# Kernel optimization log

Hardware: AMD Instinct MI355X
Metric: run time of the kernel (lower is better)

Reference implementation:

```python
import jax, jax.numpy as jnp
import numpy as np

B, S, T, D, V, H = 8, 256, 128, 768, 50257, 12
HD = D // H
TAU = 0.5
RATE = 1.0
PARAM1, PARAM2 = 0.0, 1.0  # n_step=0 => param2=1, param1=0 (update happens after use)
NEG = -1e9


def gru_cell(x, h, w_ih, w_hh, b_ih, b_hh):
    # torch nn.GRU cell math
    gi = x @ w_ih.T + b_ih   # [B,3D]
    gh = h @ w_hh.T + b_hh   # [B,3D]
    i_r, i_z, i_n = jnp.split(gi, 3, axis=-1)
    h_r, h_z, h_n = jnp.split(gh, 3, axis=-1)
    r = jax.nn.sigmoid(i_r + h_r)
    z = jax.nn.sigmoid(i_z + h_z)
    n = jnp.tanh(i_n + r * h_n)
    return (1.0 - z) * n + z * h


def gru_scan(x_btd, h0, lens, w_ih, w_hh, b_ih, b_hh):
    # emulates packed GRU: hidden frozen past each length, outputs zero past length
    x_tbd = jnp.swapaxes(x_btd, 0, 1)
    ts = jnp.arange(x_tbd.shape[0])
    def step(h, xt_t):
        xt, t = xt_t
        hn = gru_cell(xt, h, w_ih, w_hh, b_ih, b_hh)
        valid = (t < lens)[:, None]
        hn = jnp.where(valid, hn, h)
        out = jnp.where(valid, hn, 0.0)
        return hn, out
    hT, outs = jax.lax.scan(step, h0, (x_tbd, ts))
    return hT, jnp.swapaxes(outs, 0, 1)


def decay_attn(tgt, mem, mem_lens, in_w, in_b, ow, ob):
    # nn.MultiheadAttention with key_padding_mask; y = tgt + rate*attn(tgt, mem, mem)
    b, s, _ = tgt.shape
    t = mem.shape[1]
    q = (tgt @ in_w[:D].T + in_b[:D]).reshape(b, s, H, HD)
    k = (mem @ in_w[D:2 * D].T + in_b[D:2 * D]).reshape(b, t, H, HD)
    v = (mem @ in_w[2 * D:].T + in_b[2 * D:]).reshape(b, t, H, HD)
    scores = jnp.einsum('bshd,bthd->bhst', q, k) / np.sqrt(HD)
    pad = jnp.arange(t)[None, :] >= mem_lens[:, None]  # True at padding
    scores = jnp.where(pad[:, None, None, :], NEG, scores)
    a = jax.nn.softmax(scores, axis=-1)
    o = jnp.einsum('bhst,bthd->bshd', a, v).reshape(b, s, D)
    o = o @ ow.T + ob
    return tgt + RATE * o


def setup_inputs() -> dict:
    key = jax.random.key(0)
    ks = jax.random.split(key, 24)
    w = lambda k, shape: jax.random.normal(k, shape, jnp.float32) * 0.02
    src = jax.random.randint(ks[0], (B, S), 0, V)
    dst = jax.random.randint(ks[1], (B, T), 0, V)
    src_len = jax.random.randint(ks[2], (B,), 1, S + 1).at[0].set(S)
    dst_len = jax.random.randint(ks[3], (B,), 1, T + 1).at[0].set(T)
    u = jax.random.uniform(ks[4], (T - 1, B, D), jnp.float32, 1e-6, 1.0 - 1e-6)
    gumbel = -jnp.log(-jnp.log(u))
    return dict(
        src=src, src_len=src_len, dst=dst, dst_len=dst_len,
        wte=w(ks[5], (V, D)),
        enc_w_ih=w(ks[6], (3 * D, D)), enc_w_hh=w(ks[7], (3 * D, D)),
        enc_b_ih=jnp.zeros((3 * D,), jnp.float32), enc_b_hh=jnp.zeros((3 * D,), jnp.float32),
        dec_w_ih=w(ks[8], (3 * D, D)), dec_w_hh=w(ks[9], (3 * D, D)),
        dec_b_ih=jnp.zeros((3 * D,), jnp.float32), dec_b_hh=jnp.zeros((3 * D,), jnp.float32),
        out_w=w(ks[10], (V, D)), out_b=jnp.zeros((V,), jnp.float32),
        ll_w=w(ks[11], (D, D)), ll_b=jnp.zeros((D,), jnp.float32),
        attn_in_w=w(ks[12], (3 * D, D)), attn_in_b=jnp.zeros((3 * D,), jnp.float32),
        attn_out_w=w(ks[13], (D, D)), attn_out_b=jnp.zeros((D,), jnp.float32),
        gumbel=gumbel,
    )


def reference(src, src_len, dst, dst_len, wte,
              enc_w_ih, enc_w_hh, enc_b_ih, enc_b_hh,
              dec_w_ih, dec_w_hh, dec_b_ih, dec_b_hh,
              out_w, out_b, ll_w, ll_b,
              attn_in_w, attn_in_b, attn_out_w, attn_out_b, gumbel):
    src_e = wte[src]  # [B,S,D]
    dst_e = wte[dst]  # [B,T,D]

    # first encode of src (packed GRU -> final hidden)
    h_enc, _ = gru_scan(src_e, jnp.zeros((B, D), src_e.dtype), src_len,
                        enc_w_ih, enc_w_hh, enc_b_ih, enc_b_hh)

    # scheduled-sampling decode (select_rate=0 => always oracle branch)
    h0 = gru_cell(dst_e[:, 0], h_enc, dec_w_ih, dec_w_hh, dec_b_ih, dec_b_hh)
    def step(h, g):
        y_soft = jax.nn.softmax((h + g) / TAU, axis=-1)  # gumbel-softmax over D
        oracle = jnp.argmax(y_soft, axis=-1)             # ids in [0, D)
        x = wte[oracle]
        hn = gru_cell(x, h, dec_w_ih, dec_w_hh, dec_b_ih, dec_b_hh)
        return hn, hn
    _, hs = jax.lax.scan(step, h0, gumbel)
    final_output = jnp.swapaxes(jnp.concatenate([h0[None], hs], axis=0), 0, 1)  # [B,T,D]

    cand_logits = final_output @ out_w.T + out_b          # [B,T,V]
    cand = wte[jnp.argmax(cand_logits, axis=-1)]          # [B,T,D]

    c_output = decay_attn(src_e, cand, dst_len, attn_in_w, attn_in_b, attn_out_w, attn_out_b)
    c_aft = src_e @ ll_w.T + ll_b
    c_multi = PARAM1 * c_aft + PARAM2 * c_output

    h_enc2, _ = gru_scan(c_multi, jnp.zeros((B, D), c_multi.dtype), src_len,
                         enc_w_ih, enc_w_hh, enc_b_ih, enc_b_hh)
    _, dst_out = gru_scan(dst_e, h_enc2, dst_len,
                          dec_w_ih, dec_w_hh, dec_b_ih, dec_b_hh)  # [B,T,D], zero-padded
    y = dst_out @ out_w.T + out_b                          # [B,T,V]
    latent_loss = jnp.sum((c_aft - c_output) ** 2)
    return (y, latent_loss)
```

## Files before the change

kernel.cpp:

```cpp
#include <hip/hip_runtime.h>

typedef unsigned short u16;
typedef unsigned int   u32;
typedef unsigned long long u64;
typedef __attribute__((ext_vector_type(8))) short short8;
typedef __attribute__((ext_vector_type(4))) float floatx4;

#define B_ 8
#define S_ 256
#define T_ 128
#define D_ 768
#define G3 2304
#define V_ 50257
#define SCAN_BLOCKS 96

__device__ __forceinline__ u16 f2bf(float f){
  u32 u = __builtin_bit_cast(u32, f);
  u32 r = (u + 0x7fffu + ((u >> 16) & 1u)) >> 16;
  return (u16)r;
}
__device__ __forceinline__ u32 fkey(float f){
  u32 u = __builtin_bit_cast(u32, f);
  return (u & 0x80000000u) ? ~u : (u | 0x80000000u);
}

__device__ __forceinline__ float pick4(float x0, float x1, float x2, float x3, int i){
  return i == 0 ? x0 : i == 1 ? x1 : i == 2 ? x2 : x3;
}

__device__ __forceinline__ float gru_h(float gir, float giz, float gin,
                                       float hr, float hz_, float hn, float hold){
  float r = 1.f / (1.f + expf(-(gir + hr)));
  float z = 1.f / (1.f + expf(-(giz + hz_)));
  float n = tanhf(gin + r * hn);
  return (1.f - z) * n + z * hold;
}

__device__ __forceinline__ void bar_sync(int* ctr, int nb, int target){
  __syncthreads();
  if (threadIdx.x == 0){
    int c = __hip_atomic_fetch_add(ctr, 1, __ATOMIC_RELAXED, __HIP_MEMORY_SCOPE_AGENT);
    if (c + 1 < target){
      int spins = 0;
      while (__hip_atomic_load(ctr, __ATOMIC_RELAXED, __HIP_MEMORY_SCOPE_AGENT) < target){
        __builtin_amdgcn_s_sleep(1);
        if (++spins > (1 << 17)) break;
      }
    }
  }
  __syncthreads();
}

__global__ __launch_bounds__(256) void embed_kernel(
    const int* __restrict__ src, const int* __restrict__ dst, const float* __restrict__ wte,
    float* __restrict__ src_e, u16* __restrict__ src_ebf, u16* __restrict__ dst_ebf,
    u16* __restrict__ wte768_bf)
{
  int row = blockIdx.x;
  if (row < B_*S_){
    const float* wp = wte + (size_t)src[row] * D_;
    for (int c = threadIdx.x; c < D_; c += 256){
      float w = wp[c];
      src_e[(size_t)row*D_ + c] = w;
      src_ebf[(size_t)row*D_ + c] = f2bf(w);
    }
  } else if (row < B_*S_ + B_*T_){
    int r2 = row - B_*S_;
    const float* wp = wte + (size_t)dst[r2] * D_;
    for (int c = threadIdx.x; c < D_; c += 256) dst_ebf[(size_t)r2*D_ + c] = f2bf(wp[c]);
  } else {
    int r3 = row - (B_*S_ + B_*T_);
    const float* wp = wte + (size_t)r3 * D_;
    for (int c = threadIdx.x; c < D_; c += 256) wte768_bf[(size_t)r3*D_ + c] = f2bf(wp[c]);
  }
}

__global__ __launch_bounds__(256) void gemm_kernel(
    const u16* __restrict__ A, const float* __restrict__ Bm, const float* __restrict__ bias,
    float* __restrict__ outF, u16* __restrict__ outBF, const float* __restrict__ resid,
    u64* __restrict__ amax, int M, int N, int K)
{
  __shared__ __align__(16) u16 As[128][40];
  __shared__ __align__(16) u16 Bs[128][40];
  const int tid = threadIdx.x;
  const int m0 = blockIdx.y * 128, n0 = blockIdx.x * 128;
  const int lrow = tid >> 2, lk = (tid & 3) * 8;
  const int lane = tid & 63, wv = tid >> 6;
  const int wm = (wv & 1) * 64, wn = (wv >> 1) * 64;
  const int quad = lane >> 4, l16 = lane & 15;
  floatx4 acc[4][4];
  #pragma unroll
  for (int i = 0; i < 4; i++)
    #pragma unroll
    for (int jj = 0; jj < 4; jj++){
      acc[i][jj][0] = 0.f; acc[i][jj][1] = 0.f; acc[i][jj][2] = 0.f; acc[i][jj][3] = 0.f;
    }

  const int n1 = n0 + lrow;
  for (int k0 = 0; k0 < K; k0 += 32){
    __syncthreads();
    *(uint4*)&As[lrow][lk]    = *(const uint4*)(A + (size_t)(m0 + lrow)      * K + k0 + lk);
    *(uint4*)&As[lrow+64][lk] = *(const uint4*)(A + (size_t)(m0 + lrow + 64) * K + k0 + lk);
    #pragma unroll
    for (int half = 0; half < 2; half++){
      const int nr = n1 + half*64;
      short8 pk = {0,0,0,0,0,0,0,0};
      if (nr < N){
        const float4* bp = (const float4*)(Bm + (size_t)nr * K + k0 + lk);
        float4 b0 = bp[0], b1 = bp[1];
        pk[0] = (short)f2bf(b0.x); pk[1] = (short)f2bf(b0.y);
        pk[2] = (short)f2bf(b0.z); pk[3] = (short)f2bf(b0.w);
        pk[4] = (short)f2bf(b1.x); pk[5] = (short)f2bf(b1.y);
        pk[6] = (short)f2bf(b1.z); pk[7] = (short)f2bf(b1.w);
      }
      *(short8*)&Bs[lrow + half*64][lk] = pk;
    }
    __syncthreads();
    short8 af[4], bf[4];
    #pragma unroll
    for (int i = 0; i < 4; i++)  af[i] = *(const short8*)&As[wm + i*16 + l16][quad*8];
    #pragma unroll
    for (int jj = 0; jj < 4; jj++) bf[jj] = *(const short8*)&Bs[wn + jj*16 + l16][quad*8];
    #pragma unroll
    for (int i = 0; i < 4; i++)
      #pragma unroll
      for (int jj = 0; jj < 4; jj++)
        acc[i][jj] = __builtin_amdgcn_mfma_f32_16x16x32_bf16(af[i], bf[jj], acc[i][jj], 0, 0, 0);
  }

  #pragma unroll
  for (int i = 0; i < 4; i++){
    #pragma unroll
    for (int r = 0; r < 4; r++){
      const int m = m0 + wm + i*16 + quad*4 + r;
      u64 best = 0;
      #pragma unroll
      for (int jj = 0; jj < 4; jj++){
        const int n = n0 + wn + jj*16 + l16;
        if (n < N){
          float vv = acc[i][jj][r];
          if (bias)  vv += bias[n];
          if (resid) vv += resid[(size_t)m * N + n];
          if (outF)  outF[(size_t)m * N + n] = vv;
          if (outBF) outBF[(size_t)m * N + n] = f2bf(vv);
          if (amax){
            u64 p = ((u64)fkey(vv) << 32) | (u64)(0xFFFFFFFFu - (u32)n);
            if (p > best) best = p;
          }
        }
      }
      if (amax){
        #pragma unroll
        for (int msk = 1; msk < 16; msk <<= 1){
          u64 o = __shfl_xor(best, msk, 64);
          if (o > best) best = o;
        }
        if (l16 == 0) atomicMax(&amax[m], best);
      }
    }
  }
}

__global__ __launch_bounds__(256, 1) void gru_scan_kernel(
    const float* __restrict__ gi, const float* __restrict__ w_hh, const float* __restrict__ b_hh,
    const float* __restrict__ h_in, float* __restrict__ hA, float* __restrict__ hB,
    float* __restrict__ h_out, u16* __restrict__ out_bf, const int* __restrict__ lens,
    int steps, int* bar)
{
  __shared__ __align__(16) float h_lds[B_ * D_];
  const int tid = threadIdx.x, lane = tid & 63, wv = tid >> 6;
  const int grp = lane >> 5, s = lane & 31;
  const int j0 = blockIdx.x * 8 + wv * 2;
  float w[2][3][24];
  #pragma unroll
  for (int c = 0; c < 2; c++)
    #pragma unroll
    for (int g = 0; g < 3; g++){
      const float* p = w_hh + ((size_t)(g * D_ + j0 + c)) * D_ + s;
      #pragma unroll
      for (int i = 0; i < 24; i++) w[c][g][i] = p[i * 32];
    }
  const bool fin = (s < 8);
  const int fbb = s >> 1, fc = s & 1;
  const int fb = grp * 4 + fbb, fj = j0 + fc;
  const float br = b_hh[fj], bz = b_hh[D_ + fj], bn = b_hh[2 * D_ + fj];
  const int len_b = lens ? lens[fb] : 0x7fffffff;
  const int nb = gridDim.x;
  const float* cur = h_in;
  float* nxt = hA;
  int bc = 0;
  for (int t = 0; t < steps; t++){
    float g0 = 0.f, g1 = 0.f, g2 = 0.f;
    if (fin){
      const float* gp = gi + ((size_t)fb * steps + t) * G3;
      g0 = gp[fj]; g1 = gp[D_ + fj]; g2 = gp[2 * D_ + fj];
    }
    #pragma unroll
    for (int i = 0; i < 12; i++){
      const int idx = tid + i * 256;
      u64 v = __hip_atomic_load((const u64*)cur + idx, __ATOMIC_RELAXED, __HIP_MEMORY_SCOPE_AGENT);
      *((u64*)h_lds + idx) = v;
    }
    __syncthreads();
    float acc[2][3][4];
    #pragma unroll
    for (int c = 0; c < 2; c++)
      #pragma unroll
      for (int g = 0; g < 3; g++)
        #pragma unroll
        for (int bb = 0; bb < 4; bb++) acc[c][g][bb] = 0.f;
    #pragma unroll
    for (int i = 0; i < 24; i++){
      const int k = s + i * 32;
      #pragma unroll
      for (int bb = 0; bb < 4; bb++){
        const float hv = h_lds[(grp * 4 + bb) * D_ + k];
        #pragma unroll
        for (int c = 0; c < 2; c++){
          acc[c][0][bb] += w[c][0][i] * hv;
          acc[c][1][bb] += w[c][1][i] * hv;
          acc[c][2][bb] += w[c][2][i] * hv;
        }
      }
    }
    #pragma unroll
    for (int m = 1; m < 32; m <<= 1){
      #pragma unroll
      for (int c = 0; c < 2; c++)
        #pragma unroll
        for (int g = 0; g < 3; g++)
          #pragma unroll
          for (int bb = 0; bb < 4; bb++)
            acc[c][g][bb] += __shfl_xor(acc[c][g][bb], m, 64);
    }
    if (fin){
      const float sr = fc ? pick4(acc[1][0][0], acc[1][0][1], acc[1][0][2], acc[1][0][3], fbb)
                          : pick4(acc[0][0][0], acc[0][0][1], acc[0][0][2], acc[0][0][3], fbb);
      const float sz = fc ? pick4(acc[1][1][0], acc[1][1][1], acc[1][1][2], acc[1][1][3], fbb)
                          : pick4(acc[0][1][0], acc[0][1][1], acc[0][1][2], acc[0][1][3], fbb);
      const float sn = fc ? pick4(acc[1][2][0], acc[1][2][1], acc[1][2][2], acc[1][2][3], fbb)
                          : pick4(acc[0][2][0], acc[0][2][1], acc[0][2][2], acc[0][2][3], fbb);
      const float hold = h_lds[fb * D_ + fj];
      const float hn_ = gru_h(g0, g1, g2, sr + br, sz + bz, sn + bn, hold);
      const bool valid = (t < len_b);
      const float hnew = valid ? hn_ : hold;
      __hip_atomic_store(nxt + fb * D_ + fj, hnew, __ATOMIC_RELAXED, __HIP_MEMORY_SCOPE_AGENT);
      if (out_bf) out_bf[((size_t)fb * steps + t) * D_ + fj] = f2bf(valid ? hn_ : 0.f);
      if (h_out && t == steps - 1) h_out[fb * D_ + fj] = hnew;
    }
    bar_sync(bar, nb, nb * (++bc));
    const float* c2 = nxt; nxt = (nxt == hA) ? hB : hA; cur = c2;
  }
}

__global__ __launch_bounds__(256, 1) void gru_decode_kernel(
    const float* __restrict__ gi3, const float* __restrict__ E, const float* __restrict__ gumbel,
    const float* __restrict__ w_hh, const float* __restrict__ b_hh,
    const float* __restrict__ h_in, float* __restrict__ hA, float* __restrict__ hB,
    u16* __restrict__ fo_bf, int* bar)
{
  __shared__ __align__(16) float h_lds[B_ * D_];
  __shared__ int oracle[B_];
  const int tid = threadIdx.x, lane = tid & 63, wv = tid >> 6;
  const int grp = lane >> 5, s = lane & 31;
  const int j0 = blockIdx.x * 8 + wv * 2;
  float w[2][3][24];
  #pragma unroll
  for (int c = 0; c < 2; c++)
    #pragma unroll
    for (int g = 0; g < 3; g++){
      const float* p = w_hh + ((size_t)(g * D_ + j0 + c)) * D_ + s;
      #pragma unroll
      for (int i = 0; i < 24; i++) w[c][g][i] = p[i * 32];
    }
  const bool fin = (s < 8);
  const int fbb = s >> 1, fc = s & 1;
  const int fb = grp * 4 + fbb, fj = j0 + fc;
  const float br = b_hh[fj], bz = b_hh[D_ + fj], bn = b_hh[2 * D_ + fj];
  const int nb = gridDim.x;
  const float* cur = h_in;
  float* nxt = hA;
  int bc = 0;
  for (int t = 0; t < T_; t++){
    #pragma unroll
    for (int i = 0; i < 12; i++){
      const int idx = tid + i * 256;
      u64 v = __hip_atomic_load((const u64*)cur + idx, __ATOMIC_RELAXED, __HIP_MEMORY_SCOPE_AGENT);
      *((u64*)h_lds + idx) = v;
    }
    __syncthreads();
    if (t > 0){
      #pragma unroll
      for (int rep = 0; rep < 2; rep++){
        const int b = wv * 2 + rep;
        const float* gp = gumbel + ((size_t)(t - 1) * B_ + b) * D_;
        u64 best = 0;
        #pragma unroll
        for (int i = 0; i < 12; i++){
          const int d = lane + i * 64;
          const float v = h_lds[b * D_ + d] + gp[d];
          u64 p = ((u64)fkey(v) << 32) | (u64)(0xFFFFFFFFu - (u32)d);
          if (p > best) best = p;
        }
        #pragma unroll
        for (int msk = 1; msk < 64; msk <<= 1){
          u64 o = __shfl_xor(best, msk, 64);
          if (o > best) best = o;
        }
        if (lane == 0) oracle[b] = (int)(0xFFFFFFFFu - (u32)(best & 0xFFFFFFFFull));
      }
    }
    __syncthreads();
    float g0 = 0.f, g1 = 0.f, g2 = 0.f;
    if (fin){
      const float* gp = (t == 0) ? (gi3 + (size_t)fb * T_ * G3) : (E + (size_t)oracle[fb] * G3);
      g0 = gp[fj]; g1 = gp[D_ + fj]; g2 = gp[2 * D_ + fj];
    }
    float acc[2][3][4];
    #pragma unroll
    for (int c = 0; c < 2; c++)
      #pragma unroll
      for (int g = 0; g < 3; g++)
        #pragma unroll
        for (int bb = 0; bb < 4; bb++) acc[c][g][bb] = 0.f;
    #pragma unroll
    for (int i = 0; i < 24; i++){
      const int k = s + i * 32;
      #pragma unroll
      for (int bb = 0; bb < 4; bb++){
        const float hv = h_lds[(grp * 4 + bb) * D_ + k];
        #pragma unroll
        for (int c = 0; c < 2; c++){
          acc[c][0][bb] += w[c][0][i] * hv;
          acc[c][1][bb] += w[c][1][i] * hv;
          acc[c][2][bb] += w[c][2][i] * hv;
        }
      }
    }
    #pragma unroll
    for (int m = 1; m < 32; m <<= 1){
      #pragma unroll
      for (int c = 0; c < 2; c++)
        #pragma unroll
        for (int g = 0; g < 3; g++)
          #pragma unroll
          for (int bb = 0; bb < 4; bb++)
            acc[c][g][bb] += __shfl_xor(acc[c][g][bb], m, 64);
    }
    if (fin){
      const float sr = fc ? pick4(acc[1][0][0], acc[1][0][1], acc[1][0][2], acc[1][0][3], fbb)
                          : pick4(acc[0][0][0], acc[0][0][1], acc[0][0][2], acc[0][0][3], fbb);
      const float sz = fc ? pick4(acc[1][1][0], acc[1][1][1], acc[1][1][2], acc[1][1][3], fbb)
                          : pick4(acc[0][1][0], acc[0][1][1], acc[0][1][2], acc[0][1][3], fbb);
      const float sn = fc ? pick4(acc[1][2][0], acc[1][2][1], acc[1][2][2], acc[1][2][3], fbb)
                          : pick4(acc[0][2][0], acc[0][2][1], acc[0][2][2], acc[0][2][3], fbb);
      const float hold = h_lds[fb * D_ + fj];
      const float hn_ = gru_h(g0, g1, g2, sr + br, sz + bz, sn + bn, hold);
      __hip_atomic_store(nxt + fb * D_ + fj, hn_, __ATOMIC_RELAXED, __HIP_MEMORY_SCOPE_AGENT);
      fo_bf[((size_t)fb * T_ + t) * D_ + fj] = f2bf(hn_);
    }
    bar_sync(bar, nb, nb * (++bc));
    const float* c2 = nxt; nxt = (nxt == hA) ? hB : hA; cur = c2;
  }
}

__global__ __launch_bounds__(256) void cand_gather_kernel(
    const u64* __restrict__ amax, const float* __restrict__ wte, u16* __restrict__ cand_bf)
{
  int row = blockIdx.x;
  u32 n = 0xFFFFFFFFu - (u32)(amax[row] & 0xFFFFFFFFull);
  if (n >= (u32)V_) n = 0;
  const float* wp = wte + (size_t)n * D_;
  for (int c = threadIdx.x; c < D_; c += 256) cand_bf[(size_t)row*D_ + c] = f2bf(wp[c]);
}

__global__ __launch_bounds__(64) void attn_kernel(
    const float* __restrict__ q, const float* __restrict__ k, const float* __restrict__ v,
    const int* __restrict__ dlen, u16* __restrict__ ao_bf)
{
  __shared__ __align__(16) float qs[64];
  __shared__ float al[128];
  const int lane = threadIdx.x;
  const int hh = blockIdx.x, s = blockIdx.y, b = blockIdx.z;
  qs[lane] = q[((size_t)(b*S_ + s))*D_ + hh*64 + lane];
  __syncthreads();
  const int len = dlen[b];
  float sc0 = -1e9f, sc1 = -1e9f;
  #pragma unroll
  for (int r = 0; r < 2; r++){
    int t = lane + r*64;
    if (t < len){
      const float4* kp = (const float4*)(k + ((size_t)(b*T_ + t))*D_ + hh*64);
      float acc = 0.f;
      #pragma unroll
      for (int i = 0; i < 16; i++){
        float4 kv = kp[i];
        float4 qv = *((const float4*)qs + i);
        acc += qv.x*kv.x + qv.y*kv.y + qv.z*kv.z + qv.w*kv.w;
      }
      if (r == 0) sc0 = acc * 0.125f; else sc1 = acc * 0.125f;
    }
  }
  float mx = fmaxf(sc0, sc1);
  #pragma unroll
  for (int msk = 1; msk < 64; msk <<= 1) mx = fmaxf(mx, __shfl_xor(mx, msk, 64));
  float e0 = (sc0 > -1e8f) ? expf(sc0 - mx) : 0.f;
  float e1 = (sc1 > -1e8f) ? expf(sc1 - mx) : 0.f;
  float sm = e0 + e1;
  #pragma unroll
  for (int msk = 1; msk < 64; msk <<= 1) sm += __shfl_xor(sm, msk, 64);
  float inv = 1.f / sm;
  al[lane] = e0 * inv; al[lane + 64] = e1 * inv;
  __syncthreads();
  float o = 0.f;
  #pragma unroll 4
  for (int t = 0; t < T_; t++) o += al[t] * v[((size_t)(b*T_ + t))*D_ + hh*64 + lane];
  ao_bf[((size_t)(b*S_ + s))*D_ + hh*64 + lane] = f2bf(o);
}

__global__ __launch_bounds__(256) void loss_kernel(
    const float* __restrict__ a, const float* __restrict__ c, float* __restrict__ acc, int n)
{
  float s = 0.f;
  for (int i = blockIdx.x*256 + threadIdx.x; i < n; i += gridDim.x*256){
    float d = a[i] - c[i]; s += d*d;
  }
  #pragma unroll
  for (int msk = 1; msk < 64; msk <<= 1) s += __shfl_xor(s, msk, 64);
  __shared__ float ps[4];
  if ((threadIdx.x & 63) == 0) ps[threadIdx.x >> 6] = s;
  __syncthreads();
  if (threadIdx.x == 0) atomicAdd(acc, ps[0] + ps[1] + ps[2] + ps[3]);
}

__global__ void loss_write_kernel(const float* __restrict__ acc, float* __restrict__ out){
  if (threadIdx.x == 0 && blockIdx.x == 0) out[0] = *acc;
}

extern "C" void kernel_launch(void* const* d_in, const int* in_sizes, int n_in,
                              void* d_out, int out_size, void* d_ws, size_t ws_size,
                              hipStream_t stream)
{
  (void)in_sizes; (void)n_in;
  const int*   src      = (const int*)d_in[0];
  const int*   src_len  = (const int*)d_in[1];
  const int*   dst      = (const int*)d_in[2];
  const int*   dst_len  = (const int*)d_in[3];
  const float* wte      = (const float*)d_in[4];
  const float* enc_w_ih = (const float*)d_in[5];
  const float* enc_w_hh = (const float*)d_in[6];
  const float* enc_b_ih = (const float*)d_in[7];
  const float* enc_b_hh = (const float*)d_in[8];
  const float* dec_w_ih = (const float*)d_in[9];
  const float* dec_w_hh = (const float*)d_in[10];
  const float* dec_b_ih = (const float*)d_in[11];
  const float* dec_b_hh = (const float*)d_in[12];
  const float* out_w    = (const float*)d_in[13];
  const float* out_b    = (const float*)d_in[14];
  const float* ll_w     = (const float*)d_in[15];
  const float* ll_b     = (const float*)d_in[16];
  const float* attn_in_w  = (const float*)d_in[17];
  const float* attn_in_b  = (const float*)d_in[18];
  const float* attn_out_w = (const float*)d_in[19];
  const float* attn_out_b = (const float*)d_in[20];
  const float* gumbel   = (const float*)d_in[21];

  unsigned char* base = (unsigned char*)d_ws;
  size_t off = 0;
  auto alloc = [&](size_t bytes) -> void* {
    off = (off + 255) & ~(size_t)255;
    void* p = base + off; off += bytes; return p;
  };
  int*   bar      = (int*)alloc(256);
  u64*   amax     = (u64*)alloc((size_t)(B_*T_)*8);
  float* hz       = (float*)alloc((size_t)B_*D_*4);
  float* hA       = (float*)alloc((size_t)B_*D_*4);
  float* hB       = (float*)alloc((size_t)B_*D_*4);
  float* h_enc    = (float*)alloc((size_t)B_*D_*4);
  float* h_enc2   = (float*)alloc((size_t)B_*D_*4);
  float* src_e    = (float*)alloc((size_t)B_*S_*D_*4);
  u16*   src_ebf  = (u16*)alloc((size_t)B_*S_*D_*2);
  u16*   dst_ebf  = (u16*)alloc((size_t)B_*T_*D_*2);
  u16*   wte768   = (u16*)alloc((size_t)D_*D_*2);
  float* gi3      = (float*)alloc((size_t)B_*T_*G3*4);
  u16*   fo_bf    = (u16*)alloc((size_t)B_*T_*D_*2);
  u16*   cand_bf  = (u16*)alloc((size_t)B_*T_*D_*2);
  u16*   ao_bf    = (u16*)alloc((size_t)B_*S_*D_*2);
  u16*   cm_bf    = (u16*)alloc((size_t)B_*S_*D_*2);
  u16*   do_bf    = (u16*)alloc((size_t)B_*T_*D_*2);
  float* BIG      = (float*)alloc((size_t)B_*S_*G3*4);
  float* gi12  = BIG;
  float* Em    = BIG;
  float* qf    = BIG;
  float* kf    = BIG + (size_t)B_*S_*D_;
  float* vf    = kf  + (size_t)B_*T_*D_;
  float* c_out = vf  + (size_t)B_*T_*D_;
  float* c_aft = BIG;
  float* lossAcc = (float*)(bar + 8);

  const size_t needed = off;
  if (ws_size < needed) return;

  hipMemsetAsync(bar, 0, 256, stream);
  hipMemsetAsync(amax, 0, (size_t)(B_*T_)*8, stream);
  hipMemsetAsync(hz, 0, (size_t)B_*D_*4, stream);

  auto gemm = [&](const u16* A, const float* Bw, const float* bias, float* oF, u16* oB,
                  const float* resid, u64* am, int M, int N, int K){
    dim3 g((unsigned)((N + 127) / 128), (unsigned)(M / 128));
    gemm_kernel<<<g, 256, 0, stream>>>(A, Bw, bias, oF, oB, resid, am, M, N, K);
  };

  embed_kernel<<<B_*S_ + B_*T_ + D_, 256, 0, stream>>>(src, dst, wte, src_e, src_ebf,
                                                       dst_ebf, wte768);

  gemm(src_ebf, enc_w_ih, enc_b_ih, gi12, nullptr, nullptr, nullptr, B_*S_, G3, D_);
  gru_scan_kernel<<<SCAN_BLOCKS, 256, 0, stream>>>(gi12, enc_w_hh, enc_b_hh, hz, hA, hB,
                                                   h_enc, nullptr, src_len, S_, bar + 0);
  gemm(dst_ebf, dec_w_ih, dec_b_ih, gi3, nullptr, nullptr, nullptr, B_*T_, G3, D_);
  gemm(wte768, dec_w_ih, dec_b_ih, Em, nullptr, nullptr, nullptr, D_, G3, D_);
  gru_decode_kernel<<<SCAN_BLOCKS, 256, 0, stream>>>(gi3, Em, gumbel, dec_w_hh, dec_b_hh,
                                                     h_enc, hA, hB, fo_bf, bar + 2);
  gemm(fo_bf, out_w, out_b, nullptr, nullptr, nullptr, amax, B_*T_, V_, D_);
  cand_gather_kernel<<<B_*T_, 256, 0, stream>>>(amax, wte, cand_bf);
  gemm(src_ebf, attn_in_w,                    attn_in_b,        qf, nullptr, nullptr, nullptr, B_*S_, D_, D_);
  gemm(cand_bf, attn_in_w + (size_t)D_*D_,    attn_in_b + D_,   kf, nullptr, nullptr, nullptr, B_*T_, D_, D_);
  gemm(cand_bf, attn_in_w + (size_t)2*D_*D_,  attn_in_b + 2*D_, vf, nullptr, nullptr, nullptr, B_*T_, D_, D_);
  attn_kernel<<<dim3(12, S_, B_), 64, 0, stream>>>(qf, kf, vf, dst_len, ao_bf);
  gemm(ao_bf, attn_out_w, attn_out_b, c_out, cm_bf, src_e, nullptr, B_*S_, D_, D_);
  gemm(src_ebf, ll_w, ll_b, c_aft, nullptr, nullptr, nullptr, B_*S_, D_, D_);
  loss_kernel<<<1024, 256, 0, stream>>>(c_aft, c_out, lossAcc, B_*S_*D_);
  gemm(cm_bf, enc_w_ih, enc_b_ih, gi12, nullptr, nullptr, nullptr, B_*S_, G3, D_);
  gru_scan_kernel<<<SCAN_BLOCKS, 256, 0, stream>>>(gi12, enc_w_hh, enc_b_hh, hz, hA, hB,
                                                   h_enc2, nullptr, src_len, S_, bar + 4);
  gru_scan_kernel<<<SCAN_BLOCKS, 256, 0, stream>>>(gi3, dec_w_hh, dec_b_hh, h_enc2, hA, hB,
                                                   nullptr, do_bf, dst_len, T_, bar + 6);
  gemm(do_bf, out_w, out_b, (float*)d_out, nullptr, nullptr, nullptr, B_*T_, V_, D_);
  loss_write_kernel<<<1, 64, 0, stream>>>(lossAcc, (float*)d_out + (size_t)out_size - 1);
}
```

Before: 8.868 ms.

## Halve GRU scan grid with 512-thread blocks and per-block flag barrier

The persistent GRU scan and decode kernels now run 48 blocks of 512 threads, each owning 16 hidden columns, instead of 96 blocks of 256 threads. The single atomic-counter grid barrier is replaced by per-block flag slots that every block polls in parallel. Both changes aim to cut per-step grid synchronisation latency, which dominates these sequential loops. The cost is more waves per CU with register-resident weights, and a barrier workspace enlarged to hold the flags.

```diff
diff --git a/kernel.cpp b/kernel.cpp
--- a/kernel.cpp
+++ b/kernel.cpp
@@ -12,7 +12,8 @@
 #define D_ 768
 #define G3 2304
 #define V_ 50257
-#define SCAN_BLOCKS 96
+#define SCAN_BLOCKS 48
+#define SCAN_THREADS 512
 
 __device__ __forceinline__ u16 f2bf(float f){
   u32 u = __builtin_bit_cast(u32, f);
@@ -36,16 +37,16 @@
   return (1.f - z) * n + z * hold;
 }
 
-__device__ __forceinline__ void bar_sync(int* ctr, int nb, int target){
+__device__ __forceinline__ void flag_bar(int* flags, int nb, int bc){
   __syncthreads();
-  if (threadIdx.x == 0){
-    int c = __hip_atomic_fetch_add(ctr, 1, __ATOMIC_RELAXED, __HIP_MEMORY_SCOPE_AGENT);
-    if (c + 1 < target){
-      int spins = 0;
-      while (__hip_atomic_load(ctr, __ATOMIC_RELAXED, __HIP_MEMORY_SCOPE_AGENT) < target){
-        __builtin_amdgcn_s_sleep(1);
-        if (++spins > (1 << 17)) break;
-      }
+  const int tid = threadIdx.x;
+  if (tid == 0)
+    __hip_atomic_store(&flags[blockIdx.x], bc, __ATOMIC_RELAXED, __HIP_MEMORY_SCOPE_AGENT);
+  if (tid < nb){
+    int spins = 0;
+    while (__hip_atomic_load(&flags[tid], __ATOMIC_RELAXED, __HIP_MEMORY_SCOPE_AGENT) < bc){
+      __builtin_amdgcn_s_sleep(1);
+      if (++spins > (1 << 17)) break;
     }
   }
   __syncthreads();
@@ -161,16 +162,16 @@
   }
 }
 
-__global__ __launch_bounds__(256, 1) void gru_scan_kernel(
+__global__ __launch_bounds__(SCAN_THREADS, 1) void gru_scan_kernel(
     const float* __restrict__ gi, const float* __restrict__ w_hh, const float* __restrict__ b_hh,
     const float* __restrict__ h_in, float* __restrict__ hA, float* __restrict__ hB,
     float* __restrict__ h_out, u16* __restrict__ out_bf, const int* __restrict__ lens,
-    int steps, int* bar)
+    int steps, int* flags)
 {
   __shared__ __align__(16) float h_lds[B_ * D_];
   const int tid = threadIdx.x, lane = tid & 63, wv = tid >> 6;
   const int grp = lane >> 5, s = lane & 31;
-  const int j0 = blockIdx.x * 8 + wv * 2;
+  const int j0 = blockIdx.x * 16 + wv * 2;
   float w[2][3][24];
   #pragma unroll
   for (int c = 0; c < 2; c++)
@@ -188,7 +189,6 @@
   const int nb = gridDim.x;
   const float* cur = h_in;
   float* nxt = hA;
-  int bc = 0;
   for (int t = 0; t < steps; t++){
     float g0 = 0.f, g1 = 0.f, g2 = 0.f;
     if (fin){
@@ -196,8 +196,8 @@
       g0 = gp[fj]; g1 = gp[D_ + fj]; g2 = gp[2 * D_ + fj];
     }
     #pragma unroll
-    for (int i = 0; i < 12; i++){
-      const int idx = tid + i * 256;
+    for (int i = 0; i < 6; i++){
+      const int idx = tid + i * SCAN_THREADS;
       u64 v = __hip_atomic_load((const u64*)cur + idx, __ATOMIC_RELAXED, __HIP_MEMORY_SCOPE_AGENT);
       *((u64*)h_lds + idx) = v;
     }
@@ -248,22 +248,22 @@
       if (out_bf) out_bf[((size_t)fb * steps + t) * D_ + fj] = f2bf(valid ? hn_ : 0.f);
       if (h_out && t == steps - 1) h_out[fb * D_ + fj] = hnew;
     }
-    bar_sync(bar, nb, nb * (++bc));
+    flag_bar(flags, nb, t + 1);
     const float* c2 = nxt; nxt = (nxt == hA) ? hB : hA; cur = c2;
   }
 }
 
-__global__ __launch_bounds__(256, 1) void gru_decode_kernel(
+__global__ __launch_bounds__(SCAN_THREADS, 1) void gru_decode_kernel(
     const float* __restrict__ gi3, const float* __restrict__ E, const float* __restrict__ gumbel,
     const float* __restrict__ w_hh, const float* __restrict__ b_hh,
     const float* __restrict__ h_in, float* __restrict__ hA, float* __restrict__ hB,
-    u16* __restrict__ fo_bf, int* bar)
+    u16* __restrict__ fo_bf, int* flags)
 {
   __shared__ __align__(16) float h_lds[B_ * D_];
   __shared__ int oracle[B_];
   const int tid = threadIdx.x, lane = tid & 63, wv = tid >> 6;
   const int grp = lane >> 5, s = lane & 31;
-  const int j0 = blockIdx.x * 8 + wv * 2;
+  const int j0 = blockIdx.x * 16 + wv * 2;
   float w[2][3][24];
   #pragma unroll
   for (int c = 0; c < 2; c++)
@@ -280,35 +280,31 @@
   const int nb = gridDim.x;
   const float* cur = h_in;
   float* nxt = hA;
-  int bc = 0;
   for (int t = 0; t < T_; t++){
     #pragma unroll
-    for (int i = 0; i < 12; i++){
-      const int idx = tid + i * 256;
+    for (int i = 0; i < 6; i++){
+      const int idx = tid + i * SCAN_THREADS;
       u64 v = __hip_atomic_load((const u64*)cur + idx, __ATOMIC_RELAXED, __HIP_MEMORY_SCOPE_AGENT);
       *((u64*)h_lds + idx) = v;
     }
     __syncthreads();
     if (t > 0){
-      #pragma unroll
-      for (int rep = 0; rep < 2; rep++){
-        const int b = wv * 2 + rep;
-        const float* gp = gumbel + ((size_t)(t - 1) * B_ + b) * D_;
-        u64 best = 0;
-        #pragma unroll
-        for (int i = 0; i < 12; i++){
-          const int d = lane + i * 64;
-          const float v = h_lds[b * D_ + d] + gp[d];
-          u64 p = ((u64)fkey(v) << 32) | (u64)(0xFFFFFFFFu - (u32)d);
-          if (p > best) best = p;
-        }
-        #pragma unroll
-        for (int msk = 1; msk < 64; msk <<= 1){
-          u64 o = __shfl_xor(best, msk, 64);
-          if (o > best) best = o;
-        }
-        if (lane == 0) oracle[b] = (int)(0xFFFFFFFFu - (u32)(best & 0xFFFFFFFFull));
-      }
+      const int b = wv;
+      const float* gp = gumbel + ((size_t)(t - 1) * B_ + b) * D_;
+      u64 best = 0;
+      #pragma unroll
+      for (int i = 0; i < 12; i++){
+        const int d = lane + i * 64;
+        const float v = h_lds[b * D_ + d] + gp[d];
+        u64 p = ((u64)fkey(v) << 32) | (u64)(0xFFFFFFFFu - (u32)d);
+        if (p > best) best = p;
+      }
+      #pragma unroll
+      for (int msk = 1; msk < 64; msk <<= 1){
+        u64 o = __shfl_xor(best, msk, 64);
+        if (o > best) best = o;
+      }
+      if (lane == 0) oracle[b] = (int)(0xFFFFFFFFu - (u32)(best & 0xFFFFFFFFull));
     }
     __syncthreads();
     float g0 = 0.f, g1 = 0.f, g2 = 0.f;
@@ -359,7 +355,7 @@
       __hip_atomic_store(nxt + fb * D_ + fj, hn_, __ATOMIC_RELAXED, __HIP_MEMORY_SCOPE_AGENT);
       fo_bf[((size_t)fb * T_ + t) * D_ + fj] = f2bf(hn_);
     }
-    bar_sync(bar, nb, nb * (++bc));
+    flag_bar(flags, nb, t + 1);
     const float* c2 = nxt; nxt = (nxt == hA) ? hB : hA; cur = c2;
   }
 }
@@ -471,7 +467,7 @@
     off = (off + 255) & ~(size_t)255;
     void* p = base + off; off += bytes; return p;
   };
-  int*   bar      = (int*)alloc(256);
+  int*   bar      = (int*)alloc(1280);
   u64*   amax     = (u64*)alloc((size_t)(B_*T_)*8);
   float* hz       = (float*)alloc((size_t)B_*D_*4);
   float* hA       = (float*)alloc((size_t)B_*D_*4);
@@ -496,12 +492,12 @@
   float* vf    = kf  + (size_t)B_*T_*D_;
   float* c_out = vf  + (size_t)B_*T_*D_;
   float* c_aft = BIG;
-  float* lossAcc = (float*)(bar + 8);
+  float* lossAcc = (float*)(bar + 256);
 
   const size_t needed = off;
   if (ws_size < needed) return;
 
-  hipMemsetAsync(bar, 0, 256, stream);
+  hipMemsetAsync(bar, 0, 1280, stream);
   hipMemsetAsync(amax, 0, (size_t)(B_*T_)*8, stream);
   hipMemsetAsync(hz, 0, (size_t)B_*D_*4, stream);
 
@@ -515,12 +511,12 @@
                                                        dst_ebf, wte768);
 
   gemm(src_ebf, enc_w_ih, enc_b_ih, gi12, nullptr, nullptr, nullptr, B_*S_, G3, D_);
-  gru_scan_kernel<<<SCAN_BLOCKS, 256, 0, stream>>>(gi12, enc_w_hh, enc_b_hh, hz, hA, hB,
-                                                   h_enc, nullptr, src_len, S_, bar + 0);
+  gru_scan_kernel<<<SCAN_BLOCKS, SCAN_THREADS, 0, stream>>>(gi12, enc_w_hh, enc_b_hh, hz, hA, hB,
+                                                            h_enc, nullptr, src_len, S_, bar + 0);
   gemm(dst_ebf, dec_w_ih, dec_b_ih, gi3, nullptr, nullptr, nullptr, B_*T_, G3, D_);
   gemm(wte768, dec_w_ih, dec_b_ih, Em, nullptr, nullptr, nullptr, D_, G3, D_);
-  gru_decode_kernel<<<SCAN_BLOCKS, 256, 0, stream>>>(gi3, Em, gumbel, dec_w_hh, dec_b_hh,
-                                                     h_enc, hA, hB, fo_bf, bar + 2);
+  gru_decode_kernel<<<SCAN_BLOCKS, SCAN_THREADS, 0, stream>>>(gi3, Em, gumbel, dec_w_hh, dec_b_hh,
+                                                              h_enc, hA, hB, fo_bf, bar + 64);
   gemm(fo_bf, out_w, out_b, nullptr, nullptr, nullptr, amax, B_*T_, V_, D_);
   cand_gather_kernel<<<B_*T_, 256, 0, stream>>>(amax, wte, cand_bf);
   gemm(src_ebf, attn_in_w,                    attn_in_b,        qf, nullptr, nullptr, nullptr, B_*S_, D_, D_);
@@ -531,10 +527,10 @@
   gemm(src_ebf, ll_w, ll_b, c_aft, nullptr, nullptr, nullptr, B_*S_, D_, D_);
   loss_kernel<<<1024, 256, 0, stream>>>(c_aft, c_out, lossAcc, B_*S_*D_);
   gemm(cm_bf, enc_w_ih, enc_b_ih, gi12, nullptr, nullptr, nullptr, B_*S_, G3, D_);
-  gru_scan_kernel<<<SCAN_BLOCKS, 256, 0, stream>>>(gi12, enc_w_hh, enc_b_hh, hz, hA, hB,
-                                                   h_enc2, nullptr, src_len, S_, bar + 4);
-  gru_scan_kernel<<<SCAN_BLOCKS, 256, 0, stream>>>(gi3, dec_w_hh, dec_b_hh, h_enc2, hA, hB,
-                                                   nullptr, do_bf, dst_len, T_, bar + 6);
+  gru_scan_kernel<<<SCAN_BLOCKS, SCAN_THREADS, 0, stream>>>(gi12, enc_w_hh, enc_b_hh, hz, hA, hB,
+                                                            h_enc2, nullptr, src_len, S_, bar + 128);
+  gru_scan_kernel<<<SCAN_BLOCKS, SCAN_THREADS, 0, stream>>>(gi3, dec_w_hh, dec_b_hh, h_enc2, hA, hB,
+                                                            nullptr, do_bf, dst_len, T_, bar + 192);
   gemm(do_bf, out_w, out_b, (float*)d_out, nullptr, nullptr, nullptr, B_*T_, V_, D_);
   loss_write_kernel<<<1, 64, 0, stream>>>(lossAcc, (float*)d_out + (size_t)out_size - 1);
 }
```

Result: no change. 8.723 ms (-1.6%).
